# Performance work log

Measured on AMD Instinct MI355X. Metric: run time of the kernel, lower is better.

## Reference

```python
import jax, jax.numpy as jnp
import numpy as np
from jax import lax

SPATIAL = 4
PAD = 1
STRIDE = 1


def _route(x, rconv_w, rconv_b, fc_w, fc_b, num_experts):
    # x: (b, c, h, w); adaptive avg pool to (SPATIAL, SPATIAL) -- h,w divisible by SPATIAL
    b, c, h, w = x.shape
    pooled = x.reshape(b, c, SPATIAL, h // SPATIAL, SPATIAL, w // SPATIAL).mean(axis=(3, 5))
    # 1x1 conv: (b,c,s,s) x (rc,c) -> (b,rc,s,s)
    y = jnp.einsum('bcij,rc->brij', pooled, rconv_w) + rconv_b[None, :, None, None]
    y = jax.nn.relu(y).reshape(b, -1)                      # (b, rc*s*s)
    y = jax.nn.relu(y @ fc_w.T + fc_b)                     # (b, num_experts*c)
    y = y.reshape(b, num_experts, c)
    return jax.nn.sigmoid(y)                               # (b, k, c)


def _conv_per_sample(xi, wi):
    # xi: (c_in, h, w), wi: (c_out, c_in, kh, kw)
    out = lax.conv_general_dilated(
        xi[None], wi, window_strides=(STRIDE, STRIDE),
        padding=[(PAD, PAD), (PAD, PAD)],
        dimension_numbers=('NCHW', 'OIHW', 'NCHW'))
    return out[0]


def setup_inputs() -> dict:
    key = jax.random.key(0)
    ks = jax.random.split(key, 6)
    b, c_in, c_out, kk, ne = 16, 256, 256, 3, 3
    rc = max(c_in // 16, 16)  # reduction_channels = 16
    x = jax.random.normal(ks[0], (b, c_in, 64, 64), dtype=jnp.float32)
    expert_weight = jax.random.normal(ks[1], (ne, c_out, c_in, kk, kk), dtype=jnp.float32) * 0.02
    rconv_w = jax.random.normal(ks[2], (rc, c_in), dtype=jnp.float32) * 0.05
    rconv_b = jax.random.normal(ks[3], (rc,), dtype=jnp.float32) * 0.05
    fc_w = jax.random.normal(ks[4], (ne * c_in, rc * SPATIAL * SPATIAL), dtype=jnp.float32) * 0.05
    fc_b = jax.random.normal(ks[5], (ne * c_in,), dtype=jnp.float32) * 0.05
    return {"x": x, "expert_weight": expert_weight, "rconv_w": rconv_w,
            "rconv_b": rconv_b, "fc_w": fc_w, "fc_b": fc_b}


def reference(x, expert_weight, rconv_w, rconv_b, fc_w, fc_b):
    ne = expert_weight.shape[0]
    r = _route(x, rconv_w, rconv_b, fc_w, fc_b, ne)        # (b, k, c_in)
    # per-sample combined weights: routing scales input channels of each expert kernel
    w = jnp.einsum('bkc,kocij->bocij', r, expert_weight)    # (b, c_out, c_in, kh, kw)
    out = jax.vmap(_conv_per_sample)(x, w)                  # (b, c_out, h', w')
    return out
```

## Files before the change

### kernel.cpp

```cpp
#include <hip/hip_runtime.h>

#define B_   16
#define C_   256
#define OC_  256
#define H_   64
#define W_   64

typedef __attribute__((ext_vector_type(8))) __bf16 bf16x8;
typedef __attribute__((ext_vector_type(4))) float  f32x4;

__device__ __forceinline__ short f2bf(float f) {
    unsigned u = __float_as_uint(f);
    u += 0x7fffu + ((u >> 16) & 1u);
    return (short)(u >> 16);
}
__device__ __forceinline__ unsigned pk2(float a, float b) {
    return (unsigned(f2bf(a)) & 0xffffu) | (unsigned(f2bf(b)) << 16);
}
__device__ __forceinline__ void gll16(const void* g, void* l) {
    __builtin_amdgcn_global_load_lds(
        (const __attribute__((address_space(1))) unsigned int*)g,
        (__attribute__((address_space(3))) unsigned int*)l,
        16, 0, 0);
}

__global__ __launch_bounds__(256) void k_transpose_pool(
        const float* __restrict__ x, short* __restrict__ xt, float* __restrict__ pooled) {
    int y = blockIdx.x, b = blockIdx.y, t = threadIdx.x;
    int si = y >> 4;
    int lane = t & 63, wv = t >> 6;
    int xq = lane & 15, cw = lane >> 4;
    __shared__ float tile[64 * 67];

    for (int cc = 0; cc < 4; ++cc) {
        int cbase = cc * 64;
        if (cc) __syncthreads();
        #pragma unroll
        for (int r = 0; r < 4; ++r) {
            int c_l = r * 16 + wv * 4 + cw;
            float4 v = *(const float4*)&x[(((size_t)b * C_ + cbase + c_l) * H_ + y) * W_ + xq * 4];
            float* tp = &tile[c_l * 67 + xq * 4];
            tp[0] = v.x; tp[1] = v.y; tp[2] = v.z; tp[3] = v.w;
            float s = v.x + v.y + v.z + v.w;
            s += __shfl_xor(s, 1);
            s += __shfl_xor(s, 2);
            if ((lane & 3) == 0)
                atomicAdd(&pooled[((b * 4 + si) * 4 + (xq >> 2)) * 256 + cbase + c_l], s);
        }
        __syncthreads();
        #pragma unroll
        for (int r2 = 0; r2 < 2; ++r2) {
            int u = r2 * 256 + t;
            int xx = u >> 3, cgl = u & 7;
            float f[8];
            #pragma unroll
            for (int j = 0; j < 8; ++j) f[j] = tile[(cgl * 8 + j) * 67 + xx];
            uint4 pkv;
            pkv.x = pk2(f[0], f[1]); pkv.y = pk2(f[2], f[3]);
            pkv.z = pk2(f[4], f[5]); pkv.w = pk2(f[6], f[7]);
            *(uint4*)&xt[(((size_t)b * H_ + y) * W_ + xx) * C_ + cbase + cgl * 8] = pkv;
        }
    }
}

__global__ __launch_bounds__(256) void k_route(
        const float* __restrict__ pooled, const float* __restrict__ rconv_w,
        const float* __restrict__ rconv_b, const float* __restrict__ fc_w,
        const float* __restrict__ fc_b, float* __restrict__ r_buf) {
    int b = blockIdx.x >> 2;
    int slice = blockIdx.x & 3;
    int t = threadIdx.x;
    int lane = t & 63, wv = t >> 6;
    __shared__ float pl[16][257];
    __shared__ float y1[256];

    #pragma unroll
    for (int q = 0; q < 16; ++q)
        pl[q][t] = pooled[b * 4096 + q * 256 + t] * (1.0f / 256.0f);
    __syncthreads();
    {
        int rcc = t >> 4, ss = t & 15;
        float acc = rconv_b[rcc];
        #pragma unroll 8
        for (int c = 0; c < 256; ++c)
            acc += pl[ss][c] * rconv_w[rcc * 256 + c];
        y1[rcc * 16 + ss] = fmaxf(acc, 0.f);
    }
    __syncthreads();
    #pragma unroll 4
    for (int i = 0; i < 48; ++i) {
        int e = slice * 192 + wv * 48 + i;
        const float* row = fc_w + (size_t)e * 256;
        float p = y1[lane]       * row[lane]
                + y1[lane + 64]  * row[lane + 64]
                + y1[lane + 128] * row[lane + 128]
                + y1[lane + 192] * row[lane + 192];
        #pragma unroll
        for (int d = 1; d < 64; d <<= 1)
            p += __shfl_xor(p, d);
        if (lane == 0) {
            float a = fmaxf(p + fc_b[e], 0.f);
            r_buf[(size_t)b * 768 + e] = 1.f / (1.f + __expf(-a));
        }
    }
}

__global__ __launch_bounds__(256) void k_combine(
        const float* __restrict__ E, const float* __restrict__ r_buf,
        short* __restrict__ wcomb) {
    int o = blockIdx.x;
    int b0 = blockIdx.y * 4;
    int t = threadIdx.x;
    __shared__ float eT[3][2304];
    #pragma unroll
    for (int k = 0; k < 3; ++k)
        #pragma unroll
        for (int q = 0; q < 9; ++q)
            eT[k][q * 256 + t] = E[((size_t)k * OC_ + o) * 2304 + q * 256 + t];
    __syncthreads();
    int c = t;
    int ccs = (c >> 5);
    int sub = ((c >> 3) & 3) * 128 + (o & 15) * 8 + (c & 7);
    int og  = o >> 4;
    #pragma unroll
    for (int bb = 0; bb < 4; ++bb) {
        int b = b0 + bb;
        float r0 = r_buf[(size_t)b * 768 + c];
        float r1 = r_buf[(size_t)b * 768 + 256 + c];
        float r2 = r_buf[(size_t)b * 768 + 512 + c];
        short* wo = wcomb + (size_t)b * 589824;
        #pragma unroll
        for (int tap = 0; tap < 9; ++tap) {
            float v = r0 * eT[0][c * 9 + tap] + r1 * eT[1][c * 9 + tap]
                    + r2 * eT[2][c * 9 + tap];
            wo[((tap * 8 + ccs) * 16 + og) * 512 + sub] = f2bf(v);
        }
    }
}

__global__ __launch_bounds__(256, 2) void k_conv(
        const short* __restrict__ xt, const short* __restrict__ wcomb,
        float* __restrict__ out, const short* __restrict__ zbuf) {
    int lin  = blockIdx.x;
    int work = (lin & 7) * 64 + (lin >> 3);
    int b      = work >> 5;
    int o_base = ((work >> 4) & 1) * 128;
    int y0     = (work & 15) * 4;

    int t = threadIdx.x;
    int lane = t & 63, w = t >> 6;
    int quad = lane >> 4, l15 = lane & 15;

    __shared__ __align__(16) short win[6 * 64 * 64];

    int zoff = (int)(zbuf - xt);

    int woff[12];
    #pragma unroll
    for (int r = 0; r < 12; ++r) {
        int u = r * 256 + t;
        int pos = u >> 3, sp = u & 7;
        int wrow = pos >> 6, xc = pos & 63;
        int yy = y0 - 1 + wrow;
        int ss = sp ^ (xc & 7);
        woff[r] = ((unsigned)yy < 64u)
            ? ((b * 64 + yy) * 64 + xc) * 256 + ss * 8
            : zoff;
    }

    int m_base = (w & 1) * 64;
    int ry0    = (w >> 1) * 2;

    const short* pA = wcomb + (size_t)b * 589824
                    + ((o_base + m_base) >> 4) * 512 + lane * 8;

    f32x4 acc[4][8];
    #pragma unroll
    for (int i = 0; i < 4; ++i)
        #pragma unroll
        for (int j = 0; j < 8; ++j) acc[i][j] = {0.f, 0.f, 0.f, 0.f};

    for (int cc = 0; cc < 4; ++cc) {
        int ccOff = cc * 64;
        int ccA   = cc * 16384;
        #pragma unroll
        for (int r = 0; r < 12; ++r)
            gll16(xt + woff[r] + ccOff, &win[(r * 256 + w * 64) * 8]);

        bf16x8 P[2][4];
        #pragma unroll
        for (int mb = 0; mb < 4; ++mb) {
            P[0][mb] = *(const bf16x8*)(pA + ccA + mb * 512);
            P[1][mb] = *(const bf16x8*)(pA + ccA + 8192 + mb * 512);
        }
        __syncthreads();

        #pragma unroll
        for (int ph = 0; ph < 18; ++ph) {
            const int tp = ph >> 1, s = ph & 1;
            const int ti = tp / 3, tj = tp % 3;
            const int cur = ph & 1;
            int slog = s * 4 + quad;

            bf16x8 bv[8];
            #pragma unroll
            for (int nb = 0; nb < 8; ++nb) {
                int rr = nb >> 2, xq4 = nb & 3;
                int xc = xq4 * 16 + l15 + (tj - 1);
                bool ok = ((unsigned)xc < 64u);
                int xs = ok ? xc : 0;
                int wrow = ry0 + rr + ti;
                bf16x8 v = *(const bf16x8*)&win[(wrow * 64 + xs) * 64
                                                + ((slog ^ (xs & 7)) * 8)];
                bf16x8 zz = {};
                bv[nb] = ok ? v : zz;
            }
            __builtin_amdgcn_s_setprio(1);
            #pragma unroll
            for (int mb = 0; mb < 4; ++mb)
                #pragma unroll
                for (int nb = 0; nb < 8; ++nb)
                    acc[mb][nb] = __builtin_amdgcn_mfma_f32_16x16x32_bf16(
                        P[cur][mb], bv[nb], acc[mb][nb], 0, 0, 0);
            __builtin_amdgcn_s_setprio(0);

            if (ph < 16) {
                const int np = ph + 2, ntp = np >> 1, ns = np & 1;
                #pragma unroll
                for (int mb = 0; mb < 4; ++mb)
                    P[cur][mb] = *(const bf16x8*)(pA + ccA + ntp * 65536
                                                  + ns * 8192 + mb * 512);
            }
        }
        if (cc < 3) __syncthreads();
    }

    #pragma unroll
    for (int mb = 0; mb < 4; ++mb) {
        #pragma unroll
        for (int nb = 0; nb < 8; ++nb) {
            int rr = nb >> 2, xq4 = nb & 3;
            int xx = xq4 * 16 + l15;
            int yy = y0 + ry0 + rr;
            #pragma unroll
            for (int rg = 0; rg < 4; ++rg) {
                int o = o_base + m_base + mb * 16 + quad * 4 + rg;
                out[(((size_t)b * OC_ + o) * H_ + yy) * W_ + xx] = acc[mb][nb][rg];
            }
        }
    }
}

extern "C" void kernel_launch(void* const* d_in, const int* in_sizes, int n_in,
                              void* d_out, int out_size, void* d_ws, size_t ws_size,
                              hipStream_t stream) {
    const float* x       = (const float*)d_in[0];
    const float* E       = (const float*)d_in[1];
    const float* rconv_w = (const float*)d_in[2];
    const float* rconv_b = (const float*)d_in[3];
    const float* fc_w    = (const float*)d_in[4];
    const float* fc_b    = (const float*)d_in[5];
    float* out = (float*)d_out;

    char* ws = (char*)d_ws;
    short* xt     = (short*)(ws);
    short* wcomb  = (short*)(ws + 33554432);
    float* pooled = (float*)(ws + 52428800);
    short* zbuf   = (short*)(ws + 52690944);
    float* rbuf   = (float*)(ws + 52692992);

    hipMemsetAsync(pooled, 0, 262144 + 1024, stream);

    k_transpose_pool<<<dim3(64, 16), 256, 0, stream>>>(x, xt, pooled);
    k_route<<<dim3(64), 256, 0, stream>>>(pooled, rconv_w, rconv_b, fc_w, fc_b, rbuf);
    k_combine<<<dim3(256, 4), 256, 0, stream>>>(E, rbuf, wcomb);
    k_conv<<<dim3(512), 256, 0, stream>>>(xt, wcomb, out, zbuf);
}
```

Before: 256.7 us.

## Reorder conv loop by column tap to reuse LDS input fragments across row taps

```diff
diff --git a/kernel.cpp b/kernel.cpp
--- a/kernel.cpp
+++ b/kernel.cpp
@@ -120,7 +120,7 @@
     __syncthreads();
     int c = t;
     int ccs = (c >> 5);
-    int sub = ((c >> 3) & 3) * 128 + (o & 15) * 8 + (c & 7);
+    int sub = (o & 15) * 32 + ((c >> 3) & 3) * 8 + (c & 7);
     int og  = o >> 4;
     #pragma unroll
     for (int bb = 0; bb < 4; ++bb) {
@@ -172,64 +172,90 @@
     int ry0    = (w >> 1) * 2;
 
     const short* pA = wcomb + (size_t)b * 589824
-                    + ((o_base + m_base) >> 4) * 512 + lane * 8;
+                    + ((o_base + m_base) >> 4) * 512 + l15 * 32 + quad * 8;
 
     f32x4 acc[4][8];
     #pragma unroll
     for (int i = 0; i < 4; ++i)
         #pragma unroll
         for (int j = 0; j < 8; ++j) acc[i][j] = {0.f, 0.f, 0.f, 0.f};
+
+    bf16x8 A[2][12];
 
     for (int cc = 0; cc < 4; ++cc) {
         int ccOff = cc * 64;
-        int ccA   = cc * 16384;
         #pragma unroll
         for (int r = 0; r < 12; ++r)
             gll16(xt + woff[r] + ccOff, &win[(r * 256 + w * 64) * 8]);
 
-        bf16x8 P[2][4];
-        #pragma unroll
-        for (int mb = 0; mb < 4; ++mb) {
-            P[0][mb] = *(const bf16x8*)(pA + ccA + mb * 512);
-            P[1][mb] = *(const bf16x8*)(pA + ccA + 8192 + mb * 512);
+        if (cc == 0) {
+            #pragma unroll
+            for (int ti = 0; ti < 3; ++ti)
+                #pragma unroll
+                for (int mb = 0; mb < 4; ++mb) {
+                    A[0][ti * 4 + mb] = *(const bf16x8*)(pA
+                        + ((ti * 3) * 8 + 0) * 8192 + mb * 512);
+                    A[1][ti * 4 + mb] = *(const bf16x8*)(pA
+                        + ((ti * 3) * 8 + 1) * 8192 + mb * 512);
+                }
         }
         __syncthreads();
 
         #pragma unroll
-        for (int ph = 0; ph < 18; ++ph) {
-            const int tp = ph >> 1, s = ph & 1;
-            const int ti = tp / 3, tj = tp % 3;
-            const int cur = ph & 1;
-            int slog = s * 4 + quad;
-
-            bf16x8 bv[8];
-            #pragma unroll
-            for (int nb = 0; nb < 8; ++nb) {
-                int rr = nb >> 2, xq4 = nb & 3;
-                int xc = xq4 * 16 + l15 + (tj - 1);
-                bool ok = ((unsigned)xc < 64u);
-                int xs = ok ? xc : 0;
-                int wrow = ry0 + rr + ti;
-                bf16x8 v = *(const bf16x8*)&win[(wrow * 64 + xs) * 64
-                                                + ((slog ^ (xs & 7)) * 8)];
-                bf16x8 zz = {};
-                bv[nb] = ok ? v : zz;
+        for (int sp = 0; sp < 6; ++sp) {
+            const int tj = sp >> 1, s = sp & 1;
+            const int slog = s * 4 + quad;
+
+            int xsA[4], lofs[4];
+            bool okA[4];
+            #pragma unroll
+            for (int xq = 0; xq < 4; ++xq) {
+                int xc = xq * 16 + l15 + (tj - 1);
+                okA[xq] = ((unsigned)xc < 64u);
+                xsA[xq] = okA[xq] ? xc : 0;
+                lofs[xq] = (slog ^ (xsA[xq] & 7)) * 8;
             }
+            bf16x8 bv[4][4];
+            #pragma unroll
+            for (int row = 0; row < 4; ++row)
+                #pragma unroll
+                for (int xq = 0; xq < 4; ++xq) {
+                    bf16x8 v = *(const bf16x8*)&win[((ry0 + row) * 64 + xsA[xq]) * 64
+                                                    + lofs[xq]];
+                    bf16x8 zz = {};
+                    bv[row][xq] = okA[xq] ? v : zz;
+                }
+
             __builtin_amdgcn_s_setprio(1);
             #pragma unroll
-            for (int mb = 0; mb < 4; ++mb)
-                #pragma unroll
-                for (int nb = 0; nb < 8; ++nb)
-                    acc[mb][nb] = __builtin_amdgcn_mfma_f32_16x16x32_bf16(
-                        P[cur][mb], bv[nb], acc[mb][nb], 0, 0, 0);
+            for (int ti = 0; ti < 3; ++ti)
+                #pragma unroll
+                for (int mb = 0; mb < 4; ++mb)
+                    #pragma unroll
+                    for (int rr = 0; rr < 2; ++rr)
+                        #pragma unroll
+                        for (int xq = 0; xq < 4; ++xq)
+                            acc[mb][rr * 4 + xq] = __builtin_amdgcn_mfma_f32_16x16x32_bf16(
+                                A[sp & 1][ti * 4 + mb], bv[rr + ti][xq],
+                                acc[mb][rr * 4 + xq], 0, 0, 0);
             __builtin_amdgcn_s_setprio(0);
 
-            if (ph < 16) {
-                const int np = ph + 2, ntp = np >> 1, ns = np & 1;
-                #pragma unroll
-                for (int mb = 0; mb < 4; ++mb)
-                    P[cur][mb] = *(const bf16x8*)(pA + ccA + ntp * 65536
-                                                  + ns * 8192 + mb * 512);
+            if (sp < 4) {
+                const int tj2 = (sp + 2) >> 1, s2 = (sp + 2) & 1;
+                #pragma unroll
+                for (int ti = 0; ti < 3; ++ti)
+                    #pragma unroll
+                    for (int mb = 0; mb < 4; ++mb)
+                        A[sp & 1][ti * 4 + mb] = *(const bf16x8*)(pA
+                            + ((ti * 3 + tj2) * 8 + cc * 2 + s2) * 8192 + mb * 512);
+            } else if (cc < 3) {
+                const int tj2 = (sp - 4) >> 1, s2 = (sp - 4) & 1;
+                #pragma unroll
+                for (int ti = 0; ti < 3; ++ti)
+                    #pragma unroll
+                    for (int mb = 0; mb < 4; ++mb)
+                        A[sp & 1][ti * 4 + mb] = *(const bf16x8*)(pA
+                            + ((ti * 3 + tj2) * 8 + (cc + 1) * 2 + s2) * 8192 + mb * 512);
             }
         }
         if (cc < 3) __syncthreads();
```

Measured after the change: 395.9 us. +54.2%, slower.

## Pad LDS input window with zero halo columns and relayout combined weights

Applied to the files above, without the earlier changes.

```diff
diff --git a/kernel.cpp b/kernel.cpp
--- a/kernel.cpp
+++ b/kernel.cpp
@@ -109,7 +109,6 @@
         const float* __restrict__ E, const float* __restrict__ r_buf,
         short* __restrict__ wcomb) {
     int o = blockIdx.x;
-    int b0 = blockIdx.y * 4;
     int t = threadIdx.x;
     __shared__ float eT[3][2304];
     #pragma unroll
@@ -119,20 +118,24 @@
             eT[k][q * 256 + t] = E[((size_t)k * OC_ + o) * 2304 + q * 256 + t];
     __syncthreads();
     int c = t;
-    int ccs = (c >> 5);
-    int sub = ((c >> 3) & 3) * 128 + (o & 15) * 8 + (c & 7);
+    float e0[9], e1[9], e2[9];
+    #pragma unroll
+    for (int tap = 0; tap < 9; ++tap) {
+        e0[tap] = eT[0][c * 9 + tap];
+        e1[tap] = eT[1][c * 9 + tap];
+        e2[tap] = eT[2][c * 9 + tap];
+    }
+    int ccs = c >> 5;
+    int sub = (o & 15) * 32 + ((c >> 3) & 3) * 8 + (c & 7);
     int og  = o >> 4;
-    #pragma unroll
-    for (int bb = 0; bb < 4; ++bb) {
-        int b = b0 + bb;
+    for (int b = 0; b < 16; ++b) {
         float r0 = r_buf[(size_t)b * 768 + c];
         float r1 = r_buf[(size_t)b * 768 + 256 + c];
         float r2 = r_buf[(size_t)b * 768 + 512 + c];
         short* wo = wcomb + (size_t)b * 589824;
         #pragma unroll
         for (int tap = 0; tap < 9; ++tap) {
-            float v = r0 * eT[0][c * 9 + tap] + r1 * eT[1][c * 9 + tap]
-                    + r2 * eT[2][c * 9 + tap];
+            float v = r0 * e0[tap] + r1 * e1[tap] + r2 * e2[tap];
             wo[((tap * 8 + ccs) * 16 + og) * 512 + sub] = f2bf(v);
         }
     }
@@ -151,9 +154,16 @@
     int lane = t & 63, w = t >> 6;
     int quad = lane >> 4, l15 = lane & 15;
 
-    __shared__ __align__(16) short win[6 * 64 * 64];
+    __shared__ __align__(16) short win[6 * 66 * 64];
 
     int zoff = (int)(zbuf - xt);
+
+    if (t < 96) {
+        int rc = t >> 3, sp = t & 7;
+        int row = rc >> 1, col = (rc & 1) ? 65 : 0;
+        uint4 z; z.x = z.y = z.z = z.w = 0u;
+        *(uint4*)&win[((row * 66 + col) * 8 + sp) * 8] = z;
+    }
 
     int woff[12];
     #pragma unroll
@@ -162,7 +172,7 @@
         int pos = u >> 3, sp = u & 7;
         int wrow = pos >> 6, xc = pos & 63;
         int yy = y0 - 1 + wrow;
-        int ss = sp ^ (xc & 7);
+        int ss = sp ^ ((xc + 1) & 7);
         woff[r] = ((unsigned)yy < 64u)
             ? ((b * 64 + yy) * 64 + xc) * 256 + ss * 8
             : zoff;
@@ -172,7 +182,7 @@
     int ry0    = (w >> 1) * 2;
 
     const short* pA = wcomb + (size_t)b * 589824
-                    + ((o_base + m_base) >> 4) * 512 + lane * 8;
+                    + ((o_base + m_base) >> 4) * 512 + l15 * 32 + quad * 8;
 
     f32x4 acc[4][8];
     #pragma unroll
@@ -185,7 +195,8 @@
         int ccA   = cc * 16384;
         #pragma unroll
         for (int r = 0; r < 12; ++r)
-            gll16(xt + woff[r] + ccOff, &win[(r * 256 + w * 64) * 8]);
+            gll16(xt + woff[r] + ccOff,
+                  &win[(r * 256 + w * 64 + (((r * 4 + w) >> 3) << 4) + 8) * 8]);
 
         bf16x8 P[2][4];
         #pragma unroll
@@ -206,14 +217,10 @@
             #pragma unroll
             for (int nb = 0; nb < 8; ++nb) {
                 int rr = nb >> 2, xq4 = nb & 3;
-                int xc = xq4 * 16 + l15 + (tj - 1);
-                bool ok = ((unsigned)xc < 64u);
-                int xs = ok ? xc : 0;
+                int xi = xq4 * 16 + l15 + tj;
                 int wrow = ry0 + rr + ti;
-                bf16x8 v = *(const bf16x8*)&win[(wrow * 64 + xs) * 64
-                                                + ((slog ^ (xs & 7)) * 8)];
-                bf16x8 zz = {};
-                bv[nb] = ok ? v : zz;
+                bv[nb] = *(const bf16x8*)&win[((wrow * 66 + xi) * 8
+                                               + (slog ^ (xi & 7))) * 8];
             }
             __builtin_amdgcn_s_setprio(1);
             #pragma unroll
@@ -273,6 +280,6 @@
 
     k_transpose_pool<<<dim3(64, 16), 256, 0, stream>>>(x, xt, pooled);
     k_route<<<dim3(64), 256, 0, stream>>>(pooled, rconv_w, rconv_b, fc_w, fc_b, rbuf);
-    k_combine<<<dim3(256, 4), 256, 0, stream>>>(E, rbuf, wcomb);
+    k_combine<<<dim3(256), 256, 0, stream>>>(E, rbuf, wcomb);
     k_conv<<<dim3(512), 256, 0, stream>>>(xt, wcomb, out, zbuf);
 }
```

New measurement: 262.5 us. 2.3% more time.

## Rework routing FC, combine batching and combined-weight layout

Applied to the files above, without the earlier changes.

```diff
diff --git a/kernel.cpp b/kernel.cpp
--- a/kernel.cpp
+++ b/kernel.cpp
@@ -67,10 +67,8 @@
         const float* __restrict__ pooled, const float* __restrict__ rconv_w,
         const float* __restrict__ rconv_b, const float* __restrict__ fc_w,
         const float* __restrict__ fc_b, float* __restrict__ r_buf) {
-    int b = blockIdx.x >> 2;
-    int slice = blockIdx.x & 3;
+    int b = blockIdx.x;
     int t = threadIdx.x;
-    int lane = t & 63, wv = t >> 6;
     __shared__ float pl[16][257];
     __shared__ float y1[256];
 
@@ -87,21 +85,14 @@
         y1[rcc * 16 + ss] = fmaxf(acc, 0.f);
     }
     __syncthreads();
-    #pragma unroll 4
-    for (int i = 0; i < 48; ++i) {
-        int e = slice * 192 + wv * 48 + i;
-        const float* row = fc_w + (size_t)e * 256;
-        float p = y1[lane]       * row[lane]
-                + y1[lane + 64]  * row[lane + 64]
-                + y1[lane + 128] * row[lane + 128]
-                + y1[lane + 192] * row[lane + 192];
-        #pragma unroll
-        for (int d = 1; d < 64; d <<= 1)
-            p += __shfl_xor(p, d);
-        if (lane == 0) {
-            float a = fmaxf(p + fc_b[e], 0.f);
-            r_buf[(size_t)b * 768 + e] = 1.f / (1.f + __expf(-a));
-        }
+    for (int e0 = 0; e0 < 768; e0 += 256) {
+        int e = e0 + t;
+        float acc = fc_b[e];
+        #pragma unroll 8
+        for (int q = 0; q < 256; ++q)
+            acc += y1[q] * fc_w[(size_t)e * 256 + q];
+        acc = fmaxf(acc, 0.f);
+        r_buf[(size_t)b * 768 + e] = 1.f / (1.f + __expf(-acc));
     }
 }
 
@@ -109,7 +100,6 @@
         const float* __restrict__ E, const float* __restrict__ r_buf,
         short* __restrict__ wcomb) {
     int o = blockIdx.x;
-    int b0 = blockIdx.y * 4;
     int t = threadIdx.x;
     __shared__ float eT[3][2304];
     #pragma unroll
@@ -119,20 +109,24 @@
             eT[k][q * 256 + t] = E[((size_t)k * OC_ + o) * 2304 + q * 256 + t];
     __syncthreads();
     int c = t;
-    int ccs = (c >> 5);
-    int sub = ((c >> 3) & 3) * 128 + (o & 15) * 8 + (c & 7);
+    float e0[9], e1[9], e2[9];
+    #pragma unroll
+    for (int tap = 0; tap < 9; ++tap) {
+        e0[tap] = eT[0][c * 9 + tap];
+        e1[tap] = eT[1][c * 9 + tap];
+        e2[tap] = eT[2][c * 9 + tap];
+    }
+    int ccs = c >> 5;
+    int sub = (o & 15) * 32 + ((c >> 3) & 3) * 8 + (c & 7);
     int og  = o >> 4;
-    #pragma unroll
-    for (int bb = 0; bb < 4; ++bb) {
-        int b = b0 + bb;
+    for (int b = 0; b < 16; ++b) {
         float r0 = r_buf[(size_t)b * 768 + c];
         float r1 = r_buf[(size_t)b * 768 + 256 + c];
         float r2 = r_buf[(size_t)b * 768 + 512 + c];
         short* wo = wcomb + (size_t)b * 589824;
         #pragma unroll
         for (int tap = 0; tap < 9; ++tap) {
-            float v = r0 * eT[0][c * 9 + tap] + r1 * eT[1][c * 9 + tap]
-                    + r2 * eT[2][c * 9 + tap];
+            float v = r0 * e0[tap] + r1 * e1[tap] + r2 * e2[tap];
             wo[((tap * 8 + ccs) * 16 + og) * 512 + sub] = f2bf(v);
         }
     }
@@ -172,7 +166,7 @@
     int ry0    = (w >> 1) * 2;
 
     const short* pA = wcomb + (size_t)b * 589824
-                    + ((o_base + m_base) >> 4) * 512 + lane * 8;
+                    + ((o_base + m_base) >> 4) * 512 + l15 * 32 + quad * 8;
 
     f32x4 acc[4][8];
     #pragma unroll
@@ -272,7 +266,7 @@
     hipMemsetAsync(pooled, 0, 262144 + 1024, stream);
 
     k_transpose_pool<<<dim3(64, 16), 256, 0, stream>>>(x, xt, pooled);
-    k_route<<<dim3(64), 256, 0, stream>>>(pooled, rconv_w, rconv_b, fc_w, fc_b, rbuf);
-    k_combine<<<dim3(256, 4), 256, 0, stream>>>(E, rbuf, wcomb);
+    k_route<<<dim3(16), 256, 0, stream>>>(pooled, rconv_w, rconv_b, fc_w, fc_b, rbuf);
+    k_combine<<<dim3(256), 256, 0, stream>>>(E, rbuf, wcomb);
     k_conv<<<dim3(512), 256, 0, stream>>>(xt, wcomb, out, zbuf);
 }
```

Result: faster. 241.7 us (-5.8%).
